# Kernel optimization log

Measured on AMD Instinct MI355X. Metric: run time of the kernel, lower is better.

Reference implementation:

```python
import jax, jax.numpy as jnp
import numpy as np

HEIGHT, WIDTH, TEMPERATURE = 128, 128, 1.0

def make_coord(height, width):
    xs = jnp.linspace(-1.0, 1.0, width)
    ys = jnp.linspace(-1.0, 1.0, height)
    yy, xx = jnp.meshgrid(ys, xs, indexing='ij')
    return jnp.stack([xx, yy], axis=-1).reshape(-1, 2)  # [H*W, 2]

def setup_inputs() -> dict:
    key = jax.random.key(0)
    x = jax.random.normal(key, (32, 128, HEIGHT, WIDTH), dtype=jnp.float32)
    return {"x": x}

def reference(x) -> jnp.ndarray:
    B, C, H, W = x.shape
    coord = make_coord(H, W)                      # [H*W, 2]
    x_flat = x.reshape(B, C, H * W) / TEMPERATURE
    prob = jax.nn.softmax(x_flat, axis=-1)        # [B, C, H*W]
    keypoints = jnp.einsum('bcn,nk->bck', prob, coord)  # [B, C, 2]
    return keypoints
```

## Files before the change

### kernel.cpp

```cpp
#include <hip/hip_runtime.h>
#include <hip/hip_bf16.h>
#include <math.h>


#define HW 16384
#define ROWS 4096
#define THREADS 256

__global__ __launch_bounds__(THREADS)
void ess_kernel(const float* __restrict__ x, float* __restrict__ out) {
    const int row = blockIdx.x;
    const float4* p = reinterpret_cast<const float4*>(x + (size_t)row * HW);
    const int t = threadIdx.x;

    float4 v[16];
#pragma unroll
    for (int i = 0; i < 16; ++i)
        v[i] = p[i * THREADS + t];

    float m = -INFINITY;
#pragma unroll
    for (int i = 0; i < 16; ++i)
        m = fmaxf(m, fmaxf(fmaxf(v[i].x, v[i].y), fmaxf(v[i].z, v[i].w)));

#pragma unroll
    for (int off = 32; off >= 1; off >>= 1)
        m = fmaxf(m, __shfl_xor(m, off));

    const float stepc = 2.0f / 127.0f;
    const int lane4 = t * 4;
    const float xx0 = -1.0f + (float)(lane4 & 127) * stepc;
    const int y0 = lane4 >> 7;

    float s = 0.f, wx = 0.f, wy = 0.f;
#pragma unroll
    for (int i = 0; i < 16; ++i) {
        float e0 = __expf(v[i].x - m);
        float e1 = __expf(v[i].y - m);
        float e2 = __expf(v[i].z - m);
        float e3 = __expf(v[i].w - m);
        float es = (e0 + e1) + (e2 + e3);
        float yy = -1.0f + (float)(i * 8 + y0) * stepc;
        s += es;
        wy = fmaf(es, yy, wy);
        wx = fmaf(e0, xx0,             wx);
        wx = fmaf(e1, xx0 +     stepc, wx);
        wx = fmaf(e2, xx0 + 2.f*stepc, wx);
        wx = fmaf(e3, xx0 + 3.f*stepc, wx);
    }

#pragma unroll
    for (int off = 32; off >= 1; off >>= 1) {
        s  += __shfl_xor(s,  off);
        wx += __shfl_xor(wx, off);
        wy += __shfl_xor(wy, off);
    }

    __shared__ float red[4][4];
    const int wave = t >> 6;
    if ((t & 63) == 0) {
        red[wave][0] = m;
        red[wave][1] = s;
        red[wave][2] = wx;
        red[wave][3] = wy;
    }
    __syncthreads();
    if (t == 0) {
        float M = fmaxf(fmaxf(red[0][0], red[1][0]),
                        fmaxf(red[2][0], red[3][0]));
        float S = 0.f, WX = 0.f, WY = 0.f;
#pragma unroll
        for (int w2 = 0; w2 < 4; ++w2) {
            float f = __expf(red[w2][0] - M);
            S  = fmaf(red[w2][1], f, S);
            WX = fmaf(red[w2][2], f, WX);
            WY = fmaf(red[w2][3], f, WY);
        }
        out[row * 2 + 0] = WX / S;
        out[row * 2 + 1] = WY / S;
    }
}

extern "C" void kernel_launch(void* const* d_in, const int* in_sizes, int n_in,
                              void* d_out, int out_size, void* d_ws, size_t ws_size,
                              hipStream_t stream) {
    const float* x = (const float*)d_in[0];
    float* out = (float*)d_out;
    ess_kernel<<<ROWS, THREADS, 0, stream>>>(x, out);
}
```

Measured before the change: 45.64 us.

## Use per-thread online softmax with double-buffered chunked loads

Replaces the load-all-then-max-then-exp scheme with an online softmax over four chunks of four float4 loads each. The next chunk is prefetched while the current one is reduced, and the running sums are rescaled whenever the max changes. This cuts the live registers from 16 float4 to 8 and drops the wave-wide max shuffle before the exp pass. It adds rescale exps per chunk, and the compiler may already have scheduled the old loads well, so the memory-bound kernel may see little change.

After: 45.42 us. Within noise of the previous version (-0.5%).

```diff
diff --git a/kernel.cpp b/kernel.cpp
--- a/kernel.cpp
+++ b/kernel.cpp
@@ -13,42 +13,59 @@
     const float4* p = reinterpret_cast<const float4*>(x + (size_t)row * HW);
     const int t = threadIdx.x;
 
-    float4 v[16];
-#pragma unroll
-    for (int i = 0; i < 16; ++i)
-        v[i] = p[i * THREADS + t];
-
-    float m = -INFINITY;
-#pragma unroll
-    for (int i = 0; i < 16; ++i)
-        m = fmaxf(m, fmaxf(fmaxf(v[i].x, v[i].y), fmaxf(v[i].z, v[i].w)));
-
-#pragma unroll
-    for (int off = 32; off >= 1; off >>= 1)
-        m = fmaxf(m, __shfl_xor(m, off));
-
     const float stepc = 2.0f / 127.0f;
     const int lane4 = t * 4;
     const float xx0 = -1.0f + (float)(lane4 & 127) * stepc;
     const int y0 = lane4 >> 7;
 
-    float s = 0.f, wx = 0.f, wy = 0.f;
+    float m = -INFINITY, s = 0.f, wx = 0.f, wy = 0.f;
+
+    float4 cur[4], nxt[4];
 #pragma unroll
-    for (int i = 0; i < 16; ++i) {
-        float e0 = __expf(v[i].x - m);
-        float e1 = __expf(v[i].y - m);
-        float e2 = __expf(v[i].z - m);
-        float e3 = __expf(v[i].w - m);
-        float es = (e0 + e1) + (e2 + e3);
-        float yy = -1.0f + (float)(i * 8 + y0) * stepc;
-        s += es;
-        wy = fmaf(es, yy, wy);
-        wx = fmaf(e0, xx0,             wx);
-        wx = fmaf(e1, xx0 +     stepc, wx);
-        wx = fmaf(e2, xx0 + 2.f*stepc, wx);
-        wx = fmaf(e3, xx0 + 3.f*stepc, wx);
+    for (int k = 0; k < 4; ++k)
+        cur[k] = p[k * THREADS + t];
+
+#pragma unroll
+    for (int g = 0; g < 4; ++g) {
+        if (g < 3) {
+#pragma unroll
+            for (int k = 0; k < 4; ++k)
+                nxt[k] = p[((g + 1) * 4 + k) * THREADS + t];
+        }
+        float gm = -INFINITY;
+#pragma unroll
+        for (int k = 0; k < 4; ++k)
+            gm = fmaxf(gm, fmaxf(fmaxf(cur[k].x, cur[k].y),
+                                 fmaxf(cur[k].z, cur[k].w)));
+        float mn = fmaxf(m, gm);
+        float sc = __expf(m - mn);
+        s *= sc; wx *= sc; wy *= sc;
+        m = mn;
+#pragma unroll
+        for (int k = 0; k < 4; ++k) {
+            float e0 = __expf(cur[k].x - m);
+            float e1 = __expf(cur[k].y - m);
+            float e2 = __expf(cur[k].z - m);
+            float e3 = __expf(cur[k].w - m);
+            float es = (e0 + e1) + (e2 + e3);
+            float yy = -1.0f + (float)((g * 4 + k) * 8 + y0) * stepc;
+            s += es;
+            wy = fmaf(es, yy, wy);
+            wx = fmaf(e0, xx0,              wx);
+            wx = fmaf(e1, xx0 +      stepc, wx);
+            wx = fmaf(e2, xx0 + 2.f *stepc, wx);
+            wx = fmaf(e3, xx0 + 3.f *stepc, wx);
+        }
+#pragma unroll
+        for (int k = 0; k < 4; ++k) cur[k] = nxt[k];
     }
 
+    float Mw = m;
+#pragma unroll
+    for (int off = 32; off >= 1; off >>= 1)
+        Mw = fmaxf(Mw, __shfl_xor(Mw, off));
+    float c = __expf(m - Mw);
+    s *= c; wx *= c; wy *= c;
 #pragma unroll
     for (int off = 32; off >= 1; off >>= 1) {
         s  += __shfl_xor(s,  off);
@@ -59,7 +76,7 @@
     __shared__ float red[4][4];
     const int wave = t >> 6;
     if ((t & 63) == 0) {
-        red[wave][0] = m;
+        red[wave][0] = Mw;
         red[wave][1] = s;
         red[wave][2] = wx;
         red[wave][3] = wy;
```
